# Kernel tuning notes

Measured on AMD Instinct MI355X. Metric: run time of the kernel, lower is better.

## Reference

```python
import jax, jax.numpy as jnp
import numpy as np

HIDDEN = 768
HEADS = 12
HEAD_DIM = HIDDEN // HEADS  # 64


def setup_inputs() -> dict:
    key = jax.random.key(0)
    ks = jax.random.split(key, 7)
    B, S = 4, 2048
    std = 0.02
    return {
        "hidden_states": jax.random.normal(ks[0], (B, S, HIDDEN), dtype=jnp.float32),
        "attention_mask": jnp.zeros((B, 1, 1, S), dtype=jnp.float32),
        "Wq": jax.random.normal(ks[1], (HIDDEN, HIDDEN), dtype=jnp.float32) * std,
        "bq": jnp.zeros((HIDDEN,), dtype=jnp.float32),
        "Wk": jax.random.normal(ks[2], (HIDDEN, HIDDEN), dtype=jnp.float32) * std,
        "bk": jnp.zeros((HIDDEN,), dtype=jnp.float32),
        "Wv": jax.random.normal(ks[3], (HIDDEN, HIDDEN), dtype=jnp.float32) * std,
        "bv": jnp.zeros((HIDDEN,), dtype=jnp.float32),
    }


def _split_heads(x):
    # [B, S, HIDDEN] -> [B, H, S, D]
    B, S, _ = x.shape
    return x.reshape(B, S, HEADS, HEAD_DIM).transpose(0, 2, 1, 3)


def reference(hidden_states, attention_mask, Wq, bq, Wk, bk, Wv, bv):
    q = _split_heads(hidden_states @ Wq + bq)
    k = _split_heads(hidden_states @ Wk + bk)
    v = _split_heads(hidden_states @ Wv + bv)
    # [B, H, S, S] full score matrix (as in the original non-fused impl)
    scores = jnp.einsum("bhqd,bhkd->bhqk", q, k) / jnp.sqrt(
        jnp.asarray(HEAD_DIM, dtype=q.dtype)
    )
    scores = scores + attention_mask
    probs = jax.nn.softmax(scores, axis=-1)
    # dropout prob = 0.0 -> identity in eval
    ctx = jnp.einsum("bhqk,bhkd->bhqd", probs, v)
    B, H, S, D = ctx.shape
    return ctx.transpose(0, 2, 1, 3).reshape(B, S, H * D)
```

## Files before the change

kernel.cpp:

```cpp
#include <hip/hip_runtime.h>

typedef __bf16 bf16;
typedef __attribute__((ext_vector_type(8))) __bf16 bf16x8;
typedef __attribute__((ext_vector_type(4))) __bf16 bf16x4;
typedef __attribute__((ext_vector_type(4))) float f32x4;
typedef __attribute__((ext_vector_type(16))) float f32x16;
typedef __attribute__((ext_vector_type(4))) unsigned int u32x4;

#define DI __device__ __forceinline__

static constexpr int HID = 768;
static constexpr int SEQ = 2048;
static constexpr int NH  = 12;
static constexpr int HD  = 64;

DI void gload16(const void* g, void* l) {
  __builtin_amdgcn_global_load_lds(
      (const __attribute__((address_space(1))) void*)g,
      (__attribute__((address_space(3))) void*)l, 16, 0, 0);
}
DI int swz128(int row, int cb) { return row * 128 + (cb ^ ((row & 7) << 4)); }

DI unsigned cvtpk_bf16(float lo, float hi) {
  unsigned d;
  asm("v_cvt_pk_bf16_f32 %0, %1, %2" : "=v"(d) : "v"(lo), "v"(hi));
  return d;
}
DI void permswap(unsigned &a, unsigned &b) {
  asm("v_permlane32_swap_b32 %0, %1" : "+v"(a), "+v"(b));
}

__global__ void k_convert_x(const float* __restrict__ X, bf16* __restrict__ Xb, int n8) {
  int i = blockIdx.x * blockDim.x + threadIdx.x;
  if (i >= n8) return;
  const f32x4* Xv = (const f32x4*)X;
  f32x4 a = Xv[2 * i], b = Xv[2 * i + 1];
  bf16x8 o;
  o[0] = (bf16)a[0]; o[1] = (bf16)a[1]; o[2] = (bf16)a[2]; o[3] = (bf16)a[3];
  o[4] = (bf16)b[0]; o[5] = (bf16)b[1]; o[6] = (bf16)b[2]; o[7] = (bf16)b[3];
  *(bf16x8*)(Xb + (size_t)i * 8) = o;
}

__global__ void k_transpose_w(const float* __restrict__ Wq, const float* __restrict__ Wk,
                              const float* __restrict__ Wv, bf16* __restrict__ WT) {
  int z = blockIdx.z;
  const float* W = (z == 0) ? Wq : (z == 1) ? Wk : Wv;
  bf16* WTz = WT + (size_t)z * HID * HID;
  int k0 = blockIdx.x * 64, n0 = blockIdx.y * 64;
  __shared__ float t[64][65];
  int tt = threadIdx.x;
  for (int p = 0; p < 4; ++p) {
    int r = p * 16 + (tt >> 4), c4 = (tt & 15) * 4;
    f32x4 v = *(const f32x4*)(W + (size_t)(k0 + r) * HID + n0 + c4);
    t[c4 + 0][r] = v[0]; t[c4 + 1][r] = v[1]; t[c4 + 2][r] = v[2]; t[c4 + 3][r] = v[3];
  }
  __syncthreads();
  for (int p = 0; p < 4; ++p) {
    int rn = p * 16 + (tt >> 4), c4 = (tt & 15) * 4;
    bf16x4 o;
    o[0] = (bf16)t[rn][c4]; o[1] = (bf16)t[rn][c4 + 1];
    o[2] = (bf16)t[rn][c4 + 2]; o[3] = (bf16)t[rn][c4 + 3];
    *(bf16x4*)(WTz + (size_t)(n0 + rn) * HID + k0 + c4) = o;
  }
}

__global__ __launch_bounds__(256, 2)
void k_qkv_gemm(const bf16* __restrict__ Xb, const bf16* __restrict__ WT,
                const float* __restrict__ bq, const float* __restrict__ bk,
                const float* __restrict__ bv,
                bf16* __restrict__ Qb, bf16* __restrict__ Kb, bf16* __restrict__ VTb) {
  int z = blockIdx.z;
  const bf16* WTz = WT + (size_t)z * HID * HID;
  const float* bias = (z == 0) ? bq : (z == 1) ? bk : bv;

  int m0 = blockIdx.x * 128, n0 = blockIdx.y * 128;
  __shared__ char lds[32768];
  int w = threadIdx.x >> 6, l = threadIdx.x & 63;
  int wr = w >> 1, wc = w & 1;

  f32x4 acc[4][4] = {};

  for (int it = 0; it < HID / 64; ++it) {
    int k0 = it * 64;
    __syncthreads();
    for (int j = 0; j < 8; ++j) {
      int base = w * 8192 + j * 1024;
      int o = base + l * 16;
      const char* src;
      if (o < 16384) {
        int row = o >> 7;
        int cb = (o & 127) ^ ((row & 7) << 4);
        src = (const char*)(Xb + (size_t)(m0 + row) * HID + k0) + cb;
      } else {
        int o2 = o - 16384;
        int row = o2 >> 7;
        int cb = (o2 & 127) ^ ((row & 7) << 4);
        src = (const char*)(WTz + (size_t)(n0 + row) * HID + k0) + cb;
      }
      gload16(src, lds + base);
    }
    __syncthreads();

    for (int kk = 0; kk < 2; ++kk) {
      bf16x8 af[4], bfr[4];
      int cb = kk * 64 + ((l >> 4) << 4);
      for (int ms = 0; ms < 4; ++ms) {
        int row = wr * 64 + ms * 16 + (l & 15);
        af[ms] = *(const bf16x8*)(lds + swz128(row, cb));
      }
      for (int ns = 0; ns < 4; ++ns) {
        int row = wc * 64 + ns * 16 + (l & 15);
        bfr[ns] = *(const bf16x8*)(lds + 16384 + swz128(row, cb));
      }
      if (z == 2) {
        for (int ms = 0; ms < 4; ++ms)
          for (int ns = 0; ns < 4; ++ns)
            acc[ms][ns] = __builtin_amdgcn_mfma_f32_16x16x32_bf16(af[ms], bfr[ns], acc[ms][ns], 0, 0, 0);
      } else {
        for (int ms = 0; ms < 4; ++ms)
          for (int ns = 0; ns < 4; ++ns)
            acc[ms][ns] = __builtin_amdgcn_mfma_f32_16x16x32_bf16(bfr[ns], af[ms], acc[ms][ns], 0, 0, 0);
      }
    }
  }

  if (z == 2) {
    #pragma unroll
    for (int ns = 0; ns < 4; ++ns) {
      int col = n0 + wc * 64 + ns * 16 + (l & 15);
      float bvv = bias[col];
      int h = col >> 6, d = col & 63;
      #pragma unroll
      for (int ms = 0; ms < 4; ++ms) {
        int m = m0 + wr * 64 + ms * 16 + ((l >> 4) << 2);
        int bb = m >> 11, s = m & 2047;
        bf16x4 pk;
        #pragma unroll
        for (int r = 0; r < 4; ++r) pk[r] = (bf16)(acc[ms][ns][r] + bvv);
        size_t base = (size_t)(bb * NH + h) * HD * SEQ;
        size_t idx = base + (size_t)(s >> 6) * 4096 + (size_t)((s >> 3) & 7) * 512
                     + (size_t)d * 8 + (s & 7);
        *(bf16x4*)(VTb + idx) = pk;
      }
    }
  } else {
    bf16* dst = (z == 0) ? Qb : Kb;
    float scale = (z == 0) ? 0.125f : 1.0f;
    #pragma unroll
    for (int ns = 0; ns < 4; ++ns) {
      int col0 = n0 + wc * 64 + ns * 16 + ((l >> 4) << 2);
      f32x4 b4 = *(const f32x4*)(bias + col0);
      int h = col0 >> 6, d = col0 & 63;
      #pragma unroll
      for (int ms = 0; ms < 4; ++ms) {
        int m = m0 + wr * 64 + ms * 16 + (l & 15);
        int bb = m >> 11, s = m & 2047;
        bf16x4 pk;
        #pragma unroll
        for (int r = 0; r < 4; ++r)
          pk[r] = (bf16)((acc[ms][ns][r] + b4[r]) * scale);
        size_t base = (size_t)(bb * NH + h) * SEQ * HD;
        size_t idx = base + (size_t)(s >> 6) * 4096 + (size_t)(d >> 3) * 512
                     + (size_t)(s & 63) * 8 + (d & 7);
        *(bf16x4*)(dst + idx) = pk;
      }
    }
  }
}

__global__ __launch_bounds__(256, 3)
void k_attn(const bf16* __restrict__ Qb, const bf16* __restrict__ Kb,
            const bf16* __restrict__ VTb, const float* __restrict__ mask,
            float* __restrict__ out) {
  __shared__ char lds[49664];
  constexpr int NT = SEQ / 64;
  int bh = blockIdx.x;
  int b = bh / NH, h = bh % NH;
  int q0 = blockIdx.y * 128;
  int w = threadIdx.x >> 6, l = threadIdx.x & 63;
  int q = l & 31, hi = l >> 5;
  const bf16* Qp = Qb + (size_t)bh * SEQ * HD;
  const char* Kbase = (const char*)(Kb + (size_t)bh * SEQ * HD);
  const char* VTbase = (const char*)(VTb + (size_t)bh * HD * SEQ);
  const float* mb = mask + (size_t)b * SEQ;

  int sq = q0 + w * 32 + q;
  bf16x8 qf[4];
  #pragma unroll
  for (int dstep = 0; dstep < 4; ++dstep)
    qf[dstep] = *(const bf16x8*)(Qp + (size_t)(sq >> 6) * 4096
                                 + (size_t)(dstep * 2 + hi) * 512 + (sq & 63) * 8);

  f32x16 acc[2] = {};
  float psum = 0.f;

  int rbase = hi * 1024 + q * 16;

  auto stage = [&](char* buf, int kt) {
    size_t t = (size_t)kt * 8192;
    int off = w * 2048;
    #pragma unroll
    for (int j = 0; j < 2; ++j)
      gload16(Kbase + t + off + j * 1024 + l * 16, buf + off + j * 1024);
    #pragma unroll
    for (int j = 0; j < 2; ++j)
      gload16(VTbase + t + off + j * 1024 + l * 16, buf + 8192 + off + j * 1024);
  };

  char* bufA = lds;
  char* bufB = lds + 16384;
  char* bufC = lds + 32768;

  stage(bufA, 0);
  stage(bufB, 1);
  asm volatile("s_waitcnt vmcnt(4)" ::: "memory");
  __builtin_amdgcn_s_barrier();
  __builtin_amdgcn_sched_barrier(0);

  for (int kt = 0; kt < NT; ++kt) {
    f32x4 mm[2][4];
    #pragma unroll
    for (int kh = 0; kh < 2; ++kh)
      #pragma unroll
      for (int blk = 0; blk < 4; ++blk)
        mm[kh][blk] = *(const f32x4*)(mb + kt * 64 + kh * 32 + blk * 8 + hi * 4);
    __builtin_amdgcn_sched_barrier(0);

    if (kt + 2 < NT) stage(bufC, kt + 2);

    const char* Kl = bufA + rbase;
    const char* Vl = bufA + 8192 + rbase;

    #pragma unroll
    for (int kh = 0; kh < 2; ++kh) {
      bf16x8 kfh[4], vfk[4];
      #pragma unroll
      for (int dstep = 0; dstep < 4; ++dstep)
        kfh[dstep] = *(const bf16x8*)(Kl + dstep * 2048 + kh * 512);
      #pragma unroll
      for (int half = 0; half < 2; ++half)
        #pragma unroll
        for (int db = 0; db < 2; ++db)
          vfk[half * 2 + db] =
              *(const bf16x8*)(Vl + (kh * 2 + half) * 2048 + db * 512);

      f32x16 p;
      #pragma unroll
      for (int r = 0; r < 16; ++r) p[r] = mm[kh][r >> 2][r & 3];
      __builtin_amdgcn_s_setprio(1);
      #pragma unroll
      for (int dstep = 0; dstep < 4; ++dstep)
        p = __builtin_amdgcn_mfma_f32_32x32x16_bf16(kfh[dstep], qf[dstep], p, 0, 0, 0);
      __builtin_amdgcn_s_setprio(0);

      #pragma unroll
      for (int r = 0; r < 16; ++r) {
        float e = __expf(p[r]);
        p[r] = e;
        psum += e;
      }

      #pragma unroll
      for (int half = 0; half < 2; ++half) {
        int base = half * 8;
        unsigned a0 = cvtpk_bf16(p[base + 0], p[base + 1]);
        unsigned a1 = cvtpk_bf16(p[base + 2], p[base + 3]);
        unsigned a2 = cvtpk_bf16(p[base + 4], p[base + 5]);
        unsigned a3 = cvtpk_bf16(p[base + 6], p[base + 7]);
        permswap(a0, a2);
        permswap(a1, a3);
        u32x4 pk; pk[0] = a0; pk[1] = a1; pk[2] = a2; pk[3] = a3;
        bf16x8 PA = __builtin_bit_cast(bf16x8, pk);
        __builtin_amdgcn_s_setprio(1);
        #pragma unroll
        for (int db = 0; db < 2; ++db)
          acc[db] = __builtin_amdgcn_mfma_f32_32x32x16_bf16(PA, vfk[half * 2 + db], acc[db], 0, 0, 0);
        __builtin_amdgcn_s_setprio(0);
      }
    }

    if (kt < NT - 1) {
      if (kt + 2 < NT) {
        asm volatile("s_waitcnt vmcnt(4)" ::: "memory");
      } else {
        asm volatile("s_waitcnt vmcnt(0)" ::: "memory");
      }
      __builtin_amdgcn_s_barrier();
      __builtin_amdgcn_sched_barrier(0);
    }

    char* tmp = bufA; bufA = bufB; bufB = bufC; bufC = tmp;
  }

  float tot = psum + __shfl_xor(psum, 32);
  float* lsumL = (float*)(lds + 49152 + w * 128);
  if (l < 32) lsumL[l] = tot;
  __syncthreads();
  f32x4 lv[4];
  #pragma unroll
  for (int blk = 0; blk < 4; ++blk)
    lv[blk] = *(const f32x4*)(lsumL + blk * 8 + hi * 4);
  float inv[16];
  #pragma unroll
  for (int r = 0; r < 16; ++r) inv[r] = 1.0f / lv[r >> 2][r & 3];

  #pragma unroll
  for (int db = 0; db < 2; ++db)
    #pragma unroll
    for (int r = 0; r < 16; ++r) {
      int s = q0 + w * 32 + (r & 3) + 8 * (r >> 2) + 4 * hi;
      out[((size_t)(b * SEQ + s)) * HID + h * HD + db * 32 + q] = acc[db][r] * inv[r];
    }
}

extern "C" void kernel_launch(void* const* d_in, const int* in_sizes, int n_in,
                              void* d_out, int out_size, void* d_ws, size_t ws_size,
                              hipStream_t stream) {
  const float* X    = (const float*)d_in[0];
  const float* mask = (const float*)d_in[1];
  const float* Wq   = (const float*)d_in[2];
  const float* bq   = (const float*)d_in[3];
  const float* Wk   = (const float*)d_in[4];
  const float* bk   = (const float*)d_in[5];
  const float* Wv   = (const float*)d_in[6];
  const float* bv   = (const float*)d_in[7];
  float* out = (float*)d_out;
  char* ws = (char*)d_ws;

  const size_t SZ_XB = (size_t)8192 * HID * 2;
  const size_t SZ_WT = (size_t)3 * HID * HID * 2;
  const size_t SZ_M  = (size_t)4 * NH * SEQ * HD * 2;
  bf16* Xb  = (bf16*)(ws);
  bf16* WT  = (bf16*)(ws + SZ_XB);
  bf16* Qb  = (bf16*)(ws + SZ_XB + SZ_WT);
  bf16* Kb  = (bf16*)(ws + SZ_XB + SZ_WT + SZ_M);
  bf16* VTb = (bf16*)(ws + SZ_XB + SZ_WT + 2 * SZ_M);

  k_convert_x<<<3072, 256, 0, stream>>>(X, Xb, 8192 * HID / 8);
  k_transpose_w<<<dim3(12, 12, 3), 256, 0, stream>>>(Wq, Wk, Wv, WT);
  k_qkv_gemm<<<dim3(64, 6, 3), 256, 0, stream>>>(Xb, WT, bq, bk, bv, Qb, Kb, VTb);
  k_attn<<<dim3(48, 16), 256, 0, stream>>>(Qb, Kb, VTb, mask, out);
}
```

Measured before the change: 125.8 us.

## Load K/V fragments directly from global memory and remap blocks for XCD L2 locality

Removes the triple-buffered LDS staging of K and V tiles, along with its barriers. Each lane now loads its MFMA operand fragments straight from global memory, which depends on L2 and cache hits instead of explicit prefetch. Block IDs are remapped so all query tiles of a given batch-head land on the same XCD, improving L2 reuse of K/V across the blocks that share them. The change drops LDS use and synchronisation but exposes global load latency inside the inner loop and duplicates loads across waves.

```diff
diff --git a/kernel.cpp b/kernel.cpp
--- a/kernel.cpp
+++ b/kernel.cpp
@@ -172,16 +172,17 @@
 void k_attn(const bf16* __restrict__ Qb, const bf16* __restrict__ Kb,
             const bf16* __restrict__ VTb, const float* __restrict__ mask,
             float* __restrict__ out) {
-  __shared__ char lds[49664];
+  __shared__ float lsumS[128];
   constexpr int NT = SEQ / 64;
-  int bh = blockIdx.x;
+  int id = blockIdx.x + 48 * blockIdx.y;
+  int xcd = id & 7, jj = id >> 3;
+  int bh = xcd * 6 + (jj % 6);
+  int qt = jj / 6;
   int b = bh / NH, h = bh % NH;
-  int q0 = blockIdx.y * 128;
+  int q0 = qt * 128;
   int w = threadIdx.x >> 6, l = threadIdx.x & 63;
   int q = l & 31, hi = l >> 5;
   const bf16* Qp = Qb + (size_t)bh * SEQ * HD;
-  const char* Kbase = (const char*)(Kb + (size_t)bh * SEQ * HD);
-  const char* VTbase = (const char*)(VTb + (size_t)bh * HD * SEQ);
   const float* mb = mask + (size_t)b * SEQ;
 
   int sq = q0 + w * 32 + q;
@@ -191,32 +192,14 @@
     qf[dstep] = *(const bf16x8*)(Qp + (size_t)(sq >> 6) * 4096
                                  + (size_t)(dstep * 2 + hi) * 512 + (sq & 63) * 8);
 
+  const char* Kp0 = (const char*)(Kb + (size_t)bh * SEQ * HD) + hi * 1024 + q * 16;
+  const char* Kp1 = Kp0 + 4096;
+  const char* Vp0 = (const char*)(VTb + (size_t)bh * HD * SEQ) + hi * 1024 + q * 16;
+  const char* Vp1 = Vp0 + 4096;
+
   f32x16 acc[2] = {};
   float psum = 0.f;
 
-  int rbase = hi * 1024 + q * 16;
-
-  auto stage = [&](char* buf, int kt) {
-    size_t t = (size_t)kt * 8192;
-    int off = w * 2048;
-    #pragma unroll
-    for (int j = 0; j < 2; ++j)
-      gload16(Kbase + t + off + j * 1024 + l * 16, buf + off + j * 1024);
-    #pragma unroll
-    for (int j = 0; j < 2; ++j)
-      gload16(VTbase + t + off + j * 1024 + l * 16, buf + 8192 + off + j * 1024);
-  };
-
-  char* bufA = lds;
-  char* bufB = lds + 16384;
-  char* bufC = lds + 32768;
-
-  stage(bufA, 0);
-  stage(bufB, 1);
-  asm volatile("s_waitcnt vmcnt(4)" ::: "memory");
-  __builtin_amdgcn_s_barrier();
-  __builtin_amdgcn_sched_barrier(0);
-
   for (int kt = 0; kt < NT; ++kt) {
     f32x4 mm[2][4];
     #pragma unroll
@@ -224,25 +207,25 @@
       #pragma unroll
       for (int blk = 0; blk < 4; ++blk)
         mm[kh][blk] = *(const f32x4*)(mb + kt * 64 + kh * 32 + blk * 8 + hi * 4);
-    __builtin_amdgcn_sched_barrier(0);
-
-    if (kt + 2 < NT) stage(bufC, kt + 2);
-
-    const char* Kl = bufA + rbase;
-    const char* Vl = bufA + 8192 + rbase;
 
     #pragma unroll
     for (int kh = 0; kh < 2; ++kh) {
       bf16x8 kfh[4], vfk[4];
-      #pragma unroll
-      for (int dstep = 0; dstep < 4; ++dstep)
-        kfh[dstep] = *(const bf16x8*)(Kl + dstep * 2048 + kh * 512);
-      #pragma unroll
-      for (int half = 0; half < 2; ++half)
-        #pragma unroll
-        for (int db = 0; db < 2; ++db)
-          vfk[half * 2 + db] =
-              *(const bf16x8*)(Vl + (kh * 2 + half) * 2048 + db * 512);
+      kfh[0] = *(const bf16x8*)(Kp0 + 0 * 2048 + kh * 512);
+      kfh[1] = *(const bf16x8*)(Kp0 + 1 * 2048 + kh * 512);
+      kfh[2] = *(const bf16x8*)(Kp1 + 0 * 2048 + kh * 512);
+      kfh[3] = *(const bf16x8*)(Kp1 + 1 * 2048 + kh * 512);
+      if (kh == 0) {
+        vfk[0] = *(const bf16x8*)(Vp0 + 0 * 2048 + 0 * 512);
+        vfk[1] = *(const bf16x8*)(Vp0 + 0 * 2048 + 1 * 512);
+        vfk[2] = *(const bf16x8*)(Vp0 + 1 * 2048 + 0 * 512);
+        vfk[3] = *(const bf16x8*)(Vp0 + 1 * 2048 + 1 * 512);
+      } else {
+        vfk[0] = *(const bf16x8*)(Vp1 + 0 * 2048 + 0 * 512);
+        vfk[1] = *(const bf16x8*)(Vp1 + 0 * 2048 + 1 * 512);
+        vfk[2] = *(const bf16x8*)(Vp1 + 1 * 2048 + 0 * 512);
+        vfk[3] = *(const bf16x8*)(Vp1 + 1 * 2048 + 1 * 512);
+      }
 
       f32x16 p;
       #pragma unroll
@@ -279,21 +262,11 @@
       }
     }
 
-    if (kt < NT - 1) {
-      if (kt + 2 < NT) {
-        asm volatile("s_waitcnt vmcnt(4)" ::: "memory");
-      } else {
-        asm volatile("s_waitcnt vmcnt(0)" ::: "memory");
-      }
-      __builtin_amdgcn_s_barrier();
-      __builtin_amdgcn_sched_barrier(0);
-    }
-
-    char* tmp = bufA; bufA = bufB; bufB = bufC; bufC = tmp;
+    Kp0 += 8192; Kp1 += 8192; Vp0 += 8192; Vp1 += 8192;
   }
 
   float tot = psum + __shfl_xor(psum, 32);
-  float* lsumL = (float*)(lds + 49152 + w * 128);
+  float* lsumL = lsumS + w * 32;
   if (l < 32) lsumL[l] = tot;
   __syncthreads();
   f32x4 lv[4];
```

Result: slower. 133.5 us (+6.1%).
